# Kernel tuning notes

Hardware: AMD Instinct MI355X
Metric: run time of the kernel (lower is better)

Reference implementation:

```python
import jax, jax.numpy as jnp
import numpy as np

ANCHORS = np.array([[10,13],[16,30],[33,23],[30,61],[62,45],[59,119],[116,90],[156,198],[373,326]], np.float32)
SCALE = 2
STRIDE = [32, 16, 8][SCALE]
ANCH_MASK = [[6,7,8],[3,4,5],[0,1,2]][SCALE]
N_CLASSES = 91
IGNORE_THR = 0.5


def _bce(x, t):
    # BCEWithLogits, elementwise: softplus(x) - x*t
    return jax.nn.softplus(x) - x * t


def setup_inputs() -> dict:
    key = jax.random.key(0)
    k1, k2, k3, k4 = jax.random.split(key, 4)
    B, T, G = 16, 50, 64
    output = jax.random.normal(k1, (B, 3, G, G, 5 + N_CLASSES), dtype=jnp.float32) * 0.1
    cls = jax.random.randint(k2, (B, T), 0, N_CLASSES).astype(jnp.float32)
    xy = jax.random.uniform(k3, (B, T, 2), minval=0.05, maxval=0.95)
    wh = jax.random.uniform(k4, (B, T, 2), minval=0.02, maxval=0.4)
    labels = jnp.concatenate([cls[..., None], xy, wh], axis=-1)
    return {"output": output, "labels": labels}


def reference(output, labels):
    B, A, G = output.shape[0], output.shape[1], output.shape[2]
    n_ch = 5 + N_CLASSES
    all_grid = jnp.asarray(ANCHORS / STRIDE)                 # [9,2] anchors in grid units
    m_anch = all_grid[jnp.asarray(ANCH_MASK)]                # [3,2]

    # decoded predicted boxes (detached in original)
    gx = jnp.arange(G, dtype=output.dtype)
    p = jax.lax.stop_gradient(output)
    px = jax.nn.sigmoid(p[..., 0]) + gx[None, None, None, :]
    py = jax.nn.sigmoid(p[..., 1]) + gx[None, None, :, None]
    pw = jnp.exp(p[..., 2]) * m_anch[:, 0][None, :, None, None]
    ph = jnp.exp(p[..., 3]) * m_anch[:, 1][None, :, None, None]
    pred = jnp.stack([px, py, pw, ph], axis=-1).reshape(B, -1, 4)   # [B, N, 4], N = A*G*G

    tx = labels[:, :, 1] * G; ty = labels[:, :, 2] * G
    tw = labels[:, :, 3] * G; th = labels[:, :, 4] * G              # [B,T]
    valid = labels.sum(-1) > 0                                      # [B,T]

    # anchor IoU: truth (0,0,w,h) vs ref anchors (0,0,aw,ah)
    aw, ah = all_grid[:, 0], all_grid[:, 1]                         # [9]
    mw = jnp.minimum(tw[..., None], aw); mh = jnp.minimum(th[..., None], ah)
    inter_a = mw * mh * ((mw > 0) & (mh > 0))
    a_iou = inter_a / (tw[..., None] * th[..., None] + aw * ah - inter_a)   # [B,T,9]
    best_n_all = jnp.argmax(a_iou, axis=-1)
    best_n = best_n_all % 3
    in_scale = (best_n_all[..., None] == jnp.asarray(ANCH_MASK)).any(-1)
    mask_t = valid & in_scale                                       # [B,T] assigned targets

    # pred-vs-truth IoU (xywh) for ignore mask
    tb = jnp.stack([tx, ty, tw, th], axis=-1)                       # [B,T,4]
    tl = jnp.maximum(pred[:, :, None, :2] - pred[:, :, None, 2:] / 2,
                     tb[:, None, :, :2] - tb[:, None, :, 2:] / 2)
    br = jnp.minimum(pred[:, :, None, :2] + pred[:, :, None, 2:] / 2,
                     tb[:, None, :, :2] + tb[:, None, :, 2:] / 2)
    en = jnp.all(tl < br, axis=-1)
    area_i = jnp.prod(br - tl, axis=-1) * en
    area_p = pred[:, :, 2] * pred[:, :, 3]
    p_iou = area_i / (area_p[:, :, None] + (tw * th)[:, None, :] - area_i)  # [B,N,T]
    p_iou = jnp.where(valid[:, None, :], p_iou, 0.0)
    ignored = (p_iou.max(-1) > IGNORE_THR).reshape(B, A, G, G)
    obj_mask = (~ignored).astype(output.dtype)

    # scatter target assignments; invalid targets routed out-of-bounds (dropped)
    i_idx = tx.astype(jnp.int32); j_idx = ty.astype(jnp.int32)
    a_idx = best_n
    b_idx = jnp.broadcast_to(jnp.arange(B)[:, None], tx.shape)
    b_sc = jnp.where(mask_t, b_idx, B)

    obj_mask = obj_mask.at[b_sc, a_idx, j_idx, i_idx].set(1.0, mode='drop')
    tmask = jnp.zeros((B, A, G, G), output.dtype).at[b_sc, a_idx, j_idx, i_idx].set(1.0, mode='drop')
    tgt_scale = jnp.zeros((B, A, G, G), output.dtype).at[b_sc, a_idx, j_idx, i_idx].set(
        jnp.sqrt(2.0 - tw * th / (G * G)), mode='drop')

    target = jnp.zeros((B, A, G, G, n_ch), output.dtype)
    target = target.at[b_sc, a_idx, j_idx, i_idx, 0].set(tx - jnp.floor(tx), mode='drop')
    target = target.at[b_sc, a_idx, j_idx, i_idx, 1].set(ty - jnp.floor(ty), mode='drop')
    target = target.at[b_sc, a_idx, j_idx, i_idx, 2].set(jnp.log(tw / m_anch[a_idx, 0] + 1e-16), mode='drop')
    target = target.at[b_sc, a_idx, j_idx, i_idx, 3].set(jnp.log(th / m_anch[a_idx, 1] + 1e-16), mode='drop')
    target = target.at[b_sc, a_idx, j_idx, i_idx, 4].set(1.0, mode='drop')
    cls = labels[:, :, 0].astype(jnp.int32)
    target = target.at[b_sc, a_idx, j_idx, i_idx, 5 + cls].set(1.0, mode='drop')

    # masked losses (mask-weighted sums == boolean-gather + reduction='sum')
    loss_xy = jnp.sum(tmask[..., None] * _bce(output[..., 0:2], target[..., 0:2]))
    out_wh = output[..., 2:4] * tgt_scale[..., None]
    targ_wh = target[..., 2:4] * tgt_scale[..., None]
    loss_wh = jnp.sum(tmask[..., None] * (out_wh - targ_wh) ** 2) / 2
    loss_obj = jnp.sum(obj_mask * _bce(output[..., 4], target[..., 4]))
    loss_cls = jnp.sum(tmask[..., None] * _bce(output[..., 5:], target[..., 5:]))
    return loss_xy + loss_wh + loss_obj + loss_cls
```

## Files before the change

### kernel.cpp

```cpp
#include <hip/hip_runtime.h>
#include <math.h>

#define NT 50
#define NG 64
#define NCLS 91
#define NCH 96
#define CELL_BLOCKS 48
#define TGT_BLOCKS  13
#define BX (CELL_BLOCKS + TGT_BLOCKS)
#define NPART (BX * 16)

__device__ __constant__ float c_aw[9] = {1.25f, 2.0f, 4.125f, 3.75f, 7.75f, 7.375f, 14.5f, 19.5f, 46.625f};
__device__ __constant__ float c_ah[9] = {1.625f, 3.75f, 2.875f, 7.625f, 5.625f, 14.875f, 11.25f, 24.75f, 40.75f};

__device__ __forceinline__ float softplusf_fast(float x) {
    return __logf(1.0f + __expf(-fabsf(x))) + fmaxf(x, 0.0f);
}

__device__ __forceinline__ void target_match(float tw, float th, bool valid,
                                             float tx, float ty,
                                             bool& mask, int& cell, int& bn) {
    float area = tw * th;
    float best = -1.0f; int bna = 0;
    #pragma unroll
    for (int k = 0; k < 9; ++k) {
        float mw = fminf(tw, c_aw[k]);
        float mh = fminf(th, c_ah[k]);
        float inter = (mw > 0.0f && mh > 0.0f) ? mw * mh : 0.0f;
        float iou = inter / (area + c_aw[k] * c_ah[k] - inter);
        if (iou > best) { best = iou; bna = k; }
    }
    mask = valid && (bna < 3);
    bn = bna;
    cell = mask ? (bna * 4096 + ((int)ty) * 64 + (int)tx) : -1;
}

__global__ __launch_bounds__(256) void yolo_scale_loss_kernel(
        const float* __restrict__ outp, const float* __restrict__ lab,
        float* __restrict__ partials) {
    const int b    = blockIdx.y;
    const int tid  = threadIdx.x;
    const int lane = tid & 63;
    __shared__ float s_red[4];

    float block_sum_contrib;

    if (blockIdx.x < CELL_BLOCKS) {
        __shared__ float4 s_box[NT];
        __shared__ int2   s_meta[NT];

        const int idx = blockIdx.x * 256 + tid;
        const size_t base = ((size_t)b * 12288 + idx) * NCH;

        const float4 p03 = *(const float4*)(outp + base);
        const float  p4  = outp[base + 4];

        if (tid < NT) {
            const float* L = lab + (size_t)(b * NT + tid) * 5;
            float cls = L[0], x = L[1], y = L[2], w = L[3], h = L[4];
            float tx = x * NG, ty = y * NG, tw = w * NG, th = h * NG;
            bool valid = (cls + x + y + w + h) > 0.0f;
            if (!valid) { tx = ty = tw = th = 0.0f; }
            bool mask; int cell, bn;
            target_match(tw, th, valid, tx, ty, mask, cell, bn);
            float hw = tw * 0.5f, hh = th * 0.5f;
            s_box[tid]  = make_float4(tx - hw, ty - hh, tx + hw, ty + hh);
            s_meta[tid] = make_int2(__float_as_int(tw * th), cell);
        }
        __syncthreads();

        const int a = idx >> 12;
        const int j = (idx >> 6) & 63;
        const int i = idx & 63;

        float pxc = 1.0f / (1.0f + __expf(-p03.x)) + (float)i;
        float pyc = 1.0f / (1.0f + __expf(-p03.y)) + (float)j;
        float pw  = __expf(p03.z) * c_aw[a];
        float ph  = __expf(p03.w) * c_ah[a];
        float parea = pw * ph;
        float pl = pxc - pw * 0.5f, pt = pyc - ph * 0.5f;
        float pr = pxc + pw * 0.5f, pb = pyc + ph * 0.5f;

        bool ign = false, matched = false;
        #pragma unroll 5
        for (int t = 0; t < NT; ++t) {
            float4 tb = s_box[t];
            int2   m  = s_meta[t];
            float tlx = fmaxf(pl, tb.x), tly = fmaxf(pt, tb.y);
            float brx = fminf(pr, tb.z), bry = fminf(pb, tb.w);
            float iw = brx - tlx, ih = bry - tly;
            float ai = (iw > 0.0f && ih > 0.0f) ? iw * ih : 0.0f;
            float den = parea + __int_as_float(m.x) - ai;
            ign     = ign     || (ai + ai > den);
            matched = matched || (m.y == idx);
        }
        block_sum_contrib = matched ? (softplusf_fast(p4) - p4)
                                    : (ign ? 0.0f : softplusf_fast(p4));
    } else {
        const int t = (blockIdx.x - CELL_BLOCKS) * 4 + (tid >> 6);
        float lsum = 0.0f;
        if (t < NT) {
            bool mask_l = false; int cell_l = -1, bn_l = 0, cls_l = 0;
            float txl = 0, tyl = 0, twl = 0, thl = 0;
            if (lane < NT) {
                const float* L = lab + (size_t)(b * NT + lane) * 5;
                float cls = L[0], x = L[1], y = L[2], w = L[3], h = L[4];
                txl = x * NG; tyl = y * NG; twl = w * NG; thl = h * NG;
                bool valid = (cls + x + y + w + h) > 0.0f;
                target_match(twl, thl, valid, txl, tyl, mask_l, cell_l, bn_l);
                cls_l = (int)cls;
            }
            const int cell_t = __shfl(cell_l, t);
            unsigned long long same = __ballot(mask_l && (cell_l == cell_t));
            bool winner = ((same >> t) & 1ull) &&
                          ((same & ((1ull << t) - 1ull)) == 0ull);
            if (winner) {
                const float tx = __shfl(txl, t), ty = __shfl(tyl, t);
                const float tw = __shfl(twl, t), th = __shfl(thl, t);
                const int   bn = __shfl(bn_l, t), cc = __shfl(cls_l, t);
                const size_t base = ((size_t)b * 12288 + cell_t) * NCH;

                for (int c = lane; c < NCLS; c += 64) {
                    float pc = outp[base + 5 + c];
                    lsum += softplusf_fast(pc) - ((c == cc) ? pc : 0.0f);
                }
                if (lane == 0) {
                    float4 p03 = *(const float4*)(outp + base);
                    float t0 = tx - floorf(tx), t1 = ty - floorf(ty);
                    float t2 = logf(tw / c_aw[bn] + 1e-16f);
                    float t3 = logf(th / c_ah[bn] + 1e-16f);
                    float s2 = 2.0f - tw * th * (1.0f / (NG * NG));
                    lsum += softplusf_fast(p03.x) - p03.x * t0;
                    lsum += softplusf_fast(p03.y) - p03.y * t1;
                    float d2 = p03.z - t2, d3 = p03.w - t3;
                    lsum += 0.5f * s2 * (d2 * d2 + d3 * d3);
                }
            }
        }
        block_sum_contrib = lsum;
    }

    float v = block_sum_contrib;
    #pragma unroll
    for (int off = 32; off > 0; off >>= 1)
        v += __shfl_down(v, off, 64);
    if (lane == 0) s_red[tid >> 6] = v;
    __syncthreads();
    if (tid == 0)
        partials[blockIdx.y * BX + blockIdx.x] = s_red[0] + s_red[1] + s_red[2] + s_red[3];
}

__global__ __launch_bounds__(256) void final_reduce_kernel(
        const float* __restrict__ partials, float* __restrict__ out) {
    __shared__ float s_red[4];
    const int tid = threadIdx.x, lane = tid & 63;
    float v = 0.0f;
    for (int i = tid; i < NPART; i += 256) v += partials[i];
    #pragma unroll
    for (int off = 32; off > 0; off >>= 1)
        v += __shfl_down(v, off, 64);
    if (lane == 0) s_red[tid >> 6] = v;
    __syncthreads();
    if (tid == 0) out[0] = s_red[0] + s_red[1] + s_red[2] + s_red[3];
}

extern "C" void kernel_launch(void* const* d_in, const int* in_sizes, int n_in,
                              void* d_out, int out_size, void* d_ws, size_t ws_size,
                              hipStream_t stream) {
    const float* outp = (const float*)d_in[0];
    const float* lab  = (const float*)d_in[1];
    float* partials   = (float*)d_ws;
    float* res        = (float*)d_out;

    const int B = in_sizes[1] / (NT * 5);

    dim3 grid(BX, B);
    yolo_scale_loss_kernel<<<grid, 256, 0, stream>>>(outp, lab, partials);
    final_reduce_kernel<<<1, 256, 0, stream>>>(partials, res);
}
```

Before: 110.7 us.

## Split each cell's target IoU loop across two threads and precompute matched flags

Each grid cell is now handled by a pair of threads, each scanning half of the 50 targets and combining the ignore flag with a lane shuffle. This doubles the number of cell blocks. The per-iteration matched compare is replaced by a shared-memory flag table filled from the target cells. The IoU threshold test is rewritten as 3*inter > parea+tarea, dropping the select and subtraction. The goal is to cut the serial loop length per thread and raise parallelism, at the cost of redundant prediction loads and decode math in both threads of each pair.

```diff
diff --git a/kernel.cpp b/kernel.cpp
--- a/kernel.cpp
+++ b/kernel.cpp
@@ -5,7 +5,8 @@
 #define NG 64
 #define NCLS 91
 #define NCH 96
-#define CELL_BLOCKS 48
+#define CPB 128
+#define CELL_BLOCKS 96
 #define TGT_BLOCKS  13
 #define BX (CELL_BLOCKS + TGT_BLOCKS)
 #define NPART (BX * 16)
@@ -43,18 +44,23 @@
     const int lane = tid & 63;
     __shared__ float s_red[4];
 
-    float block_sum_contrib;
+    float contrib = 0.0f;
 
     if (blockIdx.x < CELL_BLOCKS) {
         __shared__ float4 s_box[NT];
-        __shared__ int2   s_meta[NT];
+        __shared__ float  s_area[NT];
+        __shared__ unsigned char s_matched[CPB];
 
-        const int idx = blockIdx.x * 256 + tid;
+        const int cell_local = tid >> 1;
+        const int half = tid & 1;
+        const int blk_start = blockIdx.x * CPB;
+        const int idx = blk_start + cell_local;
         const size_t base = ((size_t)b * 12288 + idx) * NCH;
 
         const float4 p03 = *(const float4*)(outp + base);
         const float  p4  = outp[base + 4];
 
+        if (tid < CPB) s_matched[tid] = 0;
         if (tid < NT) {
             const float* L = lab + (size_t)(b * NT + tid) * 5;
             float cls = L[0], x = L[1], y = L[2], w = L[3], h = L[4];
@@ -65,7 +71,9 @@
             target_match(tw, th, valid, tx, ty, mask, cell, bn);
             float hw = tw * 0.5f, hh = th * 0.5f;
             s_box[tid]  = make_float4(tx - hw, ty - hh, tx + hw, ty + hh);
-            s_meta[tid] = make_int2(__float_as_int(tw * th), cell);
+            s_area[tid] = tw * th;
+            if (cell >= blk_start && cell < blk_start + CPB)
+                s_matched[cell - blk_start] = 1;
         }
         __syncthreads();
 
@@ -81,24 +89,28 @@
         float pl = pxc - pw * 0.5f, pt = pyc - ph * 0.5f;
         float pr = pxc + pw * 0.5f, pb = pyc + ph * 0.5f;
 
-        bool ign = false, matched = false;
+        bool ign = false;
+        const int t0 = half * 25;
         #pragma unroll 5
-        for (int t = 0; t < NT; ++t) {
-            float4 tb = s_box[t];
-            int2   m  = s_meta[t];
+        for (int k = 0; k < 25; ++k) {
+            float4 tb = s_box[t0 + k];
+            float  ar = s_area[t0 + k];
             float tlx = fmaxf(pl, tb.x), tly = fmaxf(pt, tb.y);
             float brx = fminf(pr, tb.z), bry = fminf(pb, tb.w);
             float iw = brx - tlx, ih = bry - tly;
-            float ai = (iw > 0.0f && ih > 0.0f) ? iw * ih : 0.0f;
-            float den = parea + __int_as_float(m.x) - ai;
-            ign     = ign     || (ai + ai > den);
-            matched = matched || (m.y == idx);
+            float ai = iw * ih;
+            ign = ign || ((fminf(iw, ih) > 0.0f) && (3.0f * ai > parea + ar));
         }
-        block_sum_contrib = matched ? (softplusf_fast(p4) - p4)
-                                    : (ign ? 0.0f : softplusf_fast(p4));
+        int ign_i = ign ? 1 : 0;
+        ign_i |= __shfl_xor(ign_i, 1, 64);
+
+        if (half == 0) {
+            bool matched = (s_matched[cell_local] != 0);
+            contrib = matched ? (softplusf_fast(p4) - p4)
+                              : (ign_i ? 0.0f : softplusf_fast(p4));
+        }
     } else {
         const int t = (blockIdx.x - CELL_BLOCKS) * 4 + (tid >> 6);
-        float lsum = 0.0f;
         if (t < NT) {
             bool mask_l = false; int cell_l = -1, bn_l = 0, cls_l = 0;
             float txl = 0, tyl = 0, twl = 0, thl = 0;
@@ -120,27 +132,28 @@
                 const int   bn = __shfl(bn_l, t), cc = __shfl(cls_l, t);
                 const size_t base = ((size_t)b * 12288 + cell_t) * NCH;
 
+                float lsum = 0.0f;
                 for (int c = lane; c < NCLS; c += 64) {
                     float pc = outp[base + 5 + c];
                     lsum += softplusf_fast(pc) - ((c == cc) ? pc : 0.0f);
                 }
                 if (lane == 0) {
                     float4 p03 = *(const float4*)(outp + base);
-                    float t0 = tx - floorf(tx), t1 = ty - floorf(ty);
-                    float t2 = logf(tw / c_aw[bn] + 1e-16f);
-                    float t3 = logf(th / c_ah[bn] + 1e-16f);
+                    float tt0 = tx - floorf(tx), tt1 = ty - floorf(ty);
+                    float tt2 = logf(tw / c_aw[bn] + 1e-16f);
+                    float tt3 = logf(th / c_ah[bn] + 1e-16f);
                     float s2 = 2.0f - tw * th * (1.0f / (NG * NG));
-                    lsum += softplusf_fast(p03.x) - p03.x * t0;
-                    lsum += softplusf_fast(p03.y) - p03.y * t1;
-                    float d2 = p03.z - t2, d3 = p03.w - t3;
+                    lsum += softplusf_fast(p03.x) - p03.x * tt0;
+                    lsum += softplusf_fast(p03.y) - p03.y * tt1;
+                    float d2 = p03.z - tt2, d3 = p03.w - tt3;
                     lsum += 0.5f * s2 * (d2 * d2 + d3 * d3);
                 }
+                contrib = lsum;
             }
         }
-        block_sum_contrib = lsum;
     }
 
-    float v = block_sum_contrib;
+    float v = contrib;
     #pragma unroll
     for (int off = 32; off > 0; off >>= 1)
         v += __shfl_down(v, off, 64);
```

Result: no change. 109.4 us (-1.2%).
